# Optimization experiments

Measured on AMD Instinct MI355X. Metric: run time of the kernel, lower is better.

Reference implementation:

```python
import jax, jax.numpy as jnp
import numpy as np

H, DQS, DQP, DVS, DVP = 12, 16, 4, 16, 8
S_SCALAR = (3.0 * DQS) ** -0.5
S_POINT = (3.0 * DQP * (9.0 * 2.0 ** 0.5)) ** -0.5
S_PAIR = 3.0 ** -0.5
_OFF = np.cumsum([0, H * DQS, H * DQS, H * DVS, H * DQP * 3, H * DQP * 3, H * DVP * 3])


def _ln(x, g, b, eps=1e-5):
    mu = x.mean(-1, keepdims=True)
    var = x.var(-1, keepdims=True)
    return (x - mu) / jnp.sqrt(var + eps) * g + b


def setup_inputs() -> dict:
    B, N, D, PD = 2, 512, 384, 128
    key = jax.random.key(0)
    ks = jax.random.split(key, 12)
    node_feats = jax.random.normal(ks[0], (B, N, D), jnp.float32)
    pair_feats = jax.random.normal(ks[1], (B, N, N, PD), jnp.float32)
    mask = jnp.ones((B, N), dtype=bool)
    # random per-residue rigid frames (orthonormal rotations via QR)
    rot = jnp.linalg.qr(jax.random.normal(ks[2], (B, N, 3, 3), jnp.float32))[0]
    trans = jax.random.normal(ks[3], (B, N, 3), jnp.float32)
    dim_qkv = int(_OFF[-1])             # 1152
    dim_out = H * (PD + DVS + 4 * DVP)  # 2112
    s = 0.02
    p = dict(
        ln_s_g=jnp.ones((D,)), ln_s_b=jnp.zeros((D,)),
        ln_p_g=jnp.ones((PD,)), ln_p_b=jnp.zeros((PD,)),
        w_pair_bias=s * jax.random.normal(ks[4], (PD, H), jnp.float32),
        w_qkv=s * jax.random.normal(ks[5], (D, dim_qkv), jnp.float32),
        point_weights=jnp.full((1, H, 1, 1), float(np.log(np.e - 1.0)), jnp.float32),
        w_out=s * jax.random.normal(ks[6], (dim_out, D), jnp.float32),
        b_out=jnp.zeros((D,)),
        ln_t_g=jnp.ones((D,)), ln_t_b=jnp.zeros((D,)),
        w_ff1=s * jax.random.normal(ks[7], (D, 4 * D), jnp.float32),
        b_ff1=jnp.zeros((4 * D,)),
        w_ff2=s * jax.random.normal(ks[8], (4 * D, D), jnp.float32),
        b_ff2=jnp.zeros((D,)),
    )
    return dict(node_feats=node_feats, pair_feats=pair_feats, mask=mask,
                rot=rot, trans=trans, **p)


def reference(node_feats, pair_feats, mask, rot, trans,
              ln_s_g, ln_s_b, ln_p_g, ln_p_b, w_pair_bias, w_qkv,
              point_weights, w_out, b_out,
              ln_t_g, ln_t_b, w_ff1, b_ff1, w_ff2, b_ff2):
    b, n, d = node_feats.shape
    x = _ln(node_feats, ln_s_g, ln_s_b)
    p = _ln(pair_feats, ln_p_g, ln_p_b)
    pair_bias = jnp.einsum('bijd,dh->bhij', p, w_pair_bias)
    qkv = x @ w_qkv  # (b,n,1152)

    def heads(t, dh):
        return t.reshape(b, n, H, dh).transpose(0, 2, 1, 3)  # b h n d

    q_s = heads(qkv[..., _OFF[0]:_OFF[1]], DQS)
    k_s = heads(qkv[..., _OFF[1]:_OFF[2]], DQS)
    v_s = heads(qkv[..., _OFF[2]:_OFF[3]], DVS)

    def to_pts(t, dp):
        pts = t.reshape(b, n, H * dp, 3)
        # rigid apply: R_i @ x + t_i (global frame)
        pts = jnp.einsum('bnxy,bnpy->bnpx', rot, pts) + trans[:, :, None, :]
        return pts.reshape(b, n, H, dp, 3).transpose(0, 2, 1, 3, 4)  # b h n d 3

    q_p = to_pts(qkv[..., _OFF[3]:_OFF[4]], DQP)
    k_p = to_pts(qkv[..., _OFF[4]:_OFF[5]], DQP)
    v_p = to_pts(qkv[..., _OFF[5]:_OFF[6]], DVP)

    scalar_logits = jnp.einsum('bhid,bhjd->bhij', q_s, k_s)
    # dist attn: -sum_{d,c} (q-k)^2, expanded to avoid (b,h,n,n,d,3) intermediate
    qq = jnp.sum(q_p * q_p, axis=(-1, -2))
    kk = jnp.sum(k_p * k_p, axis=(-1, -2))
    qk = jnp.einsum('bhidc,bhjdc->bhij', q_p, k_p)
    point_logits = -(qq[..., :, None] + kk[..., None, :] - 2.0 * qk)
    point_logits = point_logits * jax.nn.softplus(point_weights)

    neg = jnp.finfo(node_feats.dtype).min
    pm = mask[:, None, :, None] & mask[:, None, None, :]  # b 1 i j
    scalar_logits = jnp.where(pm, scalar_logits, neg)
    point_logits = jnp.where(pm, point_logits, neg)
    pair_bias = jnp.where(pm, pair_bias, neg)

    logits = S_SCALAR * scalar_logits + S_POINT * point_logits + S_PAIR * pair_bias
    attn = jax.nn.softmax(logits, axis=-1)

    out_s = jnp.einsum('bhij,bhjd->bhid', attn, v_s)
    out_pair = jnp.einsum('bhij,bijd->bhid', attn, p)
    out_p = jnp.einsum('bhij,bhjdc->bhidc', attn, v_p)
    # rigid inverse: R_i^T (x - t_i) back to local frame
    pts = out_p.transpose(0, 2, 1, 3, 4).reshape(b, n, H * DVP, 3)
    pts = jnp.einsum('bnyx,bnpy->bnpx', rot, pts - trans[:, :, None, :])
    out_p = pts.reshape(b, n, H, DVP, 3)
    pnorm = jnp.sqrt(jnp.sum(out_p * out_p, axis=-1) + 1e-8)  # safe_norm

    cat = jnp.concatenate([
        out_s.transpose(0, 2, 1, 3).reshape(b, n, H * DVS),
        out_p.reshape(b, n, H * DVP * 3),
        pnorm.reshape(b, n, H * DVP),
        out_pair.transpose(0, 2, 1, 3).reshape(b, n, -1),
    ], axis=-1)
    attn_out = cat @ w_out + b_out

    # residuals + transition (dropout=0 -> identity). Note: transition is
    # applied to attn_out (pre-residual), exactly as in the torch forward.
    node1 = attn_out + node_feats
    t = _ln(attn_out, ln_t_g, ln_t_b)
    t = jax.nn.gelu(t @ w_ff1 + b_ff1) @ w_ff2 + b_ff2
    return t + node1
```

## Files before the change

kernel.cpp:

```cpp
#include <hip/hip_runtime.h>
#include <hip/hip_bf16.h>
#include <math.h>

typedef __hip_bfloat16 bf16;
typedef unsigned short ushort_t;
typedef ushort_t ushort8 __attribute__((ext_vector_type(8)));
typedef ushort_t us4 __attribute__((ext_vector_type(4)));
typedef short bf16x8 __attribute__((ext_vector_type(8)));
typedef float f32x4 __attribute__((ext_vector_type(4)));

constexpr float S_SCALAR = 0.14433756729740643f;
constexpr float S_POINT  = 0.08091531528f;
constexpr float S_PAIR   = 0.5773502691896258f;

__device__ inline float ldf(const float* p) { return *p; }
__device__ inline float ldf(const bf16* p)  { return __bfloat162float(*p); }
__device__ inline void stf(float* p, float v) { *p = v; }
__device__ inline void stf(bf16* p, float v)  { *p = __float2bfloat16(v); }

__device__ inline short f2bfs(float x) {
  return (short)__builtin_bit_cast(unsigned short, __float2bfloat16(x));
}
__device__ inline ushort_t f2bfu(float x) {
  return (ushort_t)__builtin_bit_cast(unsigned short, __float2bfloat16(x));
}

__device__ inline float gelu_tanh(float x) {
  float c = 0.7978845608028654f * (x + 0.044715f * x * x * x);
  return 0.5f * x * (1.f + tanhf(c));
}

__global__ __launch_bounds__(128) void ln384_kernel(
    const float* __restrict__ in, const float* __restrict__ g,
    const float* __restrict__ b, float* __restrict__ out)
{
  int row = blockIdx.x;
  const float* x = in + (size_t)row * 384;
  int t = threadIdx.x;
  float v[3]; float s = 0.f, s2 = 0.f;
#pragma unroll
  for (int i = 0; i < 3; i++) { v[i] = x[t + 128 * i]; s += v[i]; s2 += v[i] * v[i]; }
  for (int o = 32; o; o >>= 1) { s += __shfl_down(s, o); s2 += __shfl_down(s2, o); }
  __shared__ float sh[4];
  int wid = t >> 6, lane = t & 63;
  if (lane == 0) { sh[wid] = s; sh[2 + wid] = s2; }
  __syncthreads();
  s = sh[0] + sh[1]; s2 = sh[2] + sh[3];
  float mean = s * (1.f / 384.f);
  float var = s2 * (1.f / 384.f) - mean * mean;
  float rstd = rsqrtf(fmaxf(var, 0.f) + 1e-5f);
  float* orow = out + (size_t)row * 384;
#pragma unroll
  for (int i = 0; i < 3; i++) {
    int c = t + 128 * i;
    orow[c] = (v[i] - mean) * rstd * g[c] + b[c];
  }
}

__global__ __launch_bounds__(256) void prep_all_kernel(
    const float* __restrict__ w_qkv, const float* __restrict__ w_out,
    const float* __restrict__ w_ff1, const float* __restrict__ w_ff2,
    ushort_t* __restrict__ wqkvT, ushort_t* __restrict__ woutT,
    ushort_t* __restrict__ wff1T, ushort_t* __restrict__ wff2T,
    const float* __restrict__ g, const float* __restrict__ bb,
    const float* __restrict__ wpb, ushort_t* __restrict__ gwbT,
    float* __restrict__ gsbs)
{
  __shared__ float shmem[2048];
  int bid = blockIdx.x;
  int t = threadIdx.x;
  if (bid < 2376) {
    const float* src; ushort_t* dst; int K, N, bx, by;
    if (bid < 432)       { src = w_qkv; dst = wqkvT; K = 384;  N = 1152; bx = bid % 36;          by = bid / 36; }
    else if (bid < 1224) { src = w_out; dst = woutT; K = 2112; N = 384;  bx = (bid - 432) % 12;  by = (bid - 432) / 12; }
    else if (bid < 1800) { src = w_ff1; dst = wff1T; K = 384;  N = 1536; bx = (bid - 1224) % 48; by = (bid - 1224) / 48; }
    else                 { src = w_ff2; dst = wff2T; K = 1536; N = 384;  bx = (bid - 1800) % 12; by = (bid - 1800) / 12; }
    float (&tile)[32][33] = *reinterpret_cast<float (*)[32][33]>(shmem);
    int n0 = bx * 32, k0 = by * 32;
    int c = t & 31, r4 = (t >> 5) * 4;
#pragma unroll
    for (int i = 0; i < 4; i++)
      tile[r4 + i][c] = src[(size_t)(k0 + r4 + i) * N + n0 + c];
    __syncthreads();
#pragma unroll
    for (int i = 0; i < 4; i++)
      dst[(size_t)(n0 + r4 + i) * K + k0 + c] = f2bfu(tile[c][r4 + i]);
    return;
  }
  for (int idx = t; idx < 2048; idx += 256) {
    int h = idx >> 7, c = idx & 127;
    float v = (h < 12) ? g[c] * wpb[c * 12 + h] : 0.f;
    bf16 r = __float2bfloat16(v);
    gwbT[idx] = __builtin_bit_cast(unsigned short, r);
    shmem[idx] = __bfloat162float(r);
  }
  __syncthreads();
  if (t < 16) {
    float s = 0.f;
    for (int c = 0; c < 128; c++) s += shmem[t * 128 + c];
    gsbs[t] = s;
  } else if (t < 32) {
    int h = t - 16;
    float s = 0.f;
    if (h < 12) for (int c = 0; c < 128; c++) s = fmaf(bb[c], wpb[c * 12 + h], s);
    gsbs[t] = s;
  }
}

template <int EPI>
__global__ __launch_bounds__(256) void gemm_mfma_kernel(
    const float* __restrict__ A, const ushort_t* __restrict__ BT,
    const float* __restrict__ bias, const float* __restrict__ r1,
    const float* __restrict__ r2, float* __restrict__ C,
    int M, int Nn, int K)
{
  __shared__ ushort_t As[64][72];
  __shared__ ushort_t Bs[64][72];
  int t = threadIdx.x;
  int w = t >> 6, l = t & 63;
  int m0 = blockIdx.y * 64, n0 = blockIdx.x * 64;
  int wm = (w >> 1) * 32, wn = (w & 1) * 32;
  int lr = l & 15, lk = l >> 4;
  int sr = t >> 2, sc = (t & 3) * 16;
  f32x4 acc[2][2];
#pragma unroll
  for (int i = 0; i < 2; i++)
#pragma unroll
    for (int j = 0; j < 2; j++) acc[i][j] = (f32x4){0.f, 0.f, 0.f, 0.f};

  for (int k0 = 0; k0 < K; k0 += 64) {
    const float* Ar = A + (size_t)(m0 + sr) * K + k0 + sc;
    const ushort_t* Br = BT + (size_t)(n0 + sr) * K + k0 + sc;
    float4 a0 = *(const float4*)(Ar + 0);
    float4 a1 = *(const float4*)(Ar + 4);
    float4 a2 = *(const float4*)(Ar + 8);
    float4 a3 = *(const float4*)(Ar + 12);
    ushort8 b0 = *(const ushort8*)(Br + 0);
    ushort8 b1 = *(const ushort8*)(Br + 8);
    ushort8 u0, u1;
    u0[0] = f2bfu(a0.x); u0[1] = f2bfu(a0.y); u0[2] = f2bfu(a0.z); u0[3] = f2bfu(a0.w);
    u0[4] = f2bfu(a1.x); u0[5] = f2bfu(a1.y); u0[6] = f2bfu(a1.z); u0[7] = f2bfu(a1.w);
    u1[0] = f2bfu(a2.x); u1[1] = f2bfu(a2.y); u1[2] = f2bfu(a2.z); u1[3] = f2bfu(a2.w);
    u1[4] = f2bfu(a3.x); u1[5] = f2bfu(a3.y); u1[6] = f2bfu(a3.z); u1[7] = f2bfu(a3.w);
    *(ushort8*)&As[sr][sc] = u0;
    *(ushort8*)&As[sr][sc + 8] = u1;
    *(ushort8*)&Bs[sr][sc] = b0;
    *(ushort8*)&Bs[sr][sc + 8] = b1;
    __syncthreads();
#pragma unroll
    for (int kk = 0; kk < 2; kk++) {
      bf16x8 af0 = *(const bf16x8*)&As[wm + lr][kk * 32 + lk * 8];
      bf16x8 af1 = *(const bf16x8*)&As[wm + 16 + lr][kk * 32 + lk * 8];
      bf16x8 bf0 = *(const bf16x8*)&Bs[wn + lr][kk * 32 + lk * 8];
      bf16x8 bf1 = *(const bf16x8*)&Bs[wn + 16 + lr][kk * 32 + lk * 8];
      acc[0][0] = __builtin_amdgcn_mfma_f32_16x16x32_bf16(af0, bf0, acc[0][0], 0, 0, 0);
      acc[0][1] = __builtin_amdgcn_mfma_f32_16x16x32_bf16(af0, bf1, acc[0][1], 0, 0, 0);
      acc[1][0] = __builtin_amdgcn_mfma_f32_16x16x32_bf16(af1, bf0, acc[1][0], 0, 0, 0);
      acc[1][1] = __builtin_amdgcn_mfma_f32_16x16x32_bf16(af1, bf1, acc[1][1], 0, 0, 0);
    }
    __syncthreads();
  }
#pragma unroll
  for (int mf = 0; mf < 2; mf++) {
#pragma unroll
    for (int nf = 0; nf < 2; nf++) {
      int nn = n0 + wn + nf * 16 + lr;
      float bv = bias ? bias[nn] : 0.f;
#pragma unroll
      for (int e = 0; e < 4; e++) {
        int m = m0 + wm + mf * 16 + lk * 4 + e;
        float v = acc[mf][nf][e] + bv;
        if (EPI == 1) v = gelu_tanh(v);
        if (EPI == 2) v += r1[(size_t)m * Nn + nn] + r2[(size_t)m * Nn + nn];
        C[(size_t)m * Nn + nn] = v;
      }
    }
  }
}

__global__ __launch_bounds__(256) void points_kernel(
    const float* __restrict__ qkv, const float* __restrict__ rot,
    const float* __restrict__ trans, float* __restrict__ qpg,
    float* __restrict__ kpg, float* __restrict__ vpg,
    float* __restrict__ qq, float* __restrict__ kk)
{
  int bn = blockIdx.x;
  const float* row = qkv + (size_t)bn * 1152;
  __shared__ float R[9], T[3];
  __shared__ float qbuf[144], kbuf[144];
  int t = threadIdx.x;
  if (t < 9) R[t] = rot[bn * 9 + t];
  if (t >= 16 && t < 19) T[t - 16] = trans[bn * 3 + t - 16];
  __syncthreads();
  if (t < 192) {
    int base = (t < 48) ? (576 + t * 3) : (t < 96) ? (720 + (t - 48) * 3) : (864 + (t - 96) * 3);
    float x = row[base], y = row[base + 1], z = row[base + 2];
    float gx = R[0] * x + R[1] * y + R[2] * z + T[0];
    float gy = R[3] * x + R[4] * y + R[5] * z + T[1];
    float gz = R[6] * x + R[7] * y + R[8] * z + T[2];
    if (t < 48) {
      float* d = qpg + (size_t)bn * 144 + t * 3;
      d[0] = gx; d[1] = gy; d[2] = gz;
      qbuf[t * 3 + 0] = gx; qbuf[t * 3 + 1] = gy; qbuf[t * 3 + 2] = gz;
    } else if (t < 96) {
      int p = t - 48;
      float* d = kpg + (size_t)bn * 144 + p * 3;
      d[0] = gx; d[1] = gy; d[2] = gz;
      kbuf[p * 3 + 0] = gx; kbuf[p * 3 + 1] = gy; kbuf[p * 3 + 2] = gz;
    } else {
      int p = t - 96;
      float* d = vpg + (size_t)bn * 288 + p * 3;
      d[0] = gx; d[1] = gy; d[2] = gz;
    }
  }
  __syncthreads();
  if (t < 24) {
    int h = (t < 12) ? t : t - 12;
    const float* src = (t < 12) ? qbuf : kbuf;
    float ssum = 0.f;
#pragma unroll
    for (int d = 0; d < 12; d++) { float v = src[h * 12 + d]; ssum = fmaf(v, v, ssum); }
    if (t < 12) qq[bn * 12 + h] = ssum; else kk[bn * 12 + h] = ssum;
  }
}

__global__ __launch_bounds__(256) void kv_prep_kernel(
    const float* __restrict__ qkv, const float* __restrict__ kpg,
    const float* __restrict__ kk, const float* __restrict__ vpg,
    float* __restrict__ kpackT, ushort_t* __restrict__ vT)
{
  int bh = blockIdx.x;
  int b = bh / 12, h = bh - b * 12;
  int j = blockIdx.y * 256 + threadIdx.x;
  const float* row = qkv + (size_t)(b * 512 + j) * 1152;
  float* kt = kpackT + (size_t)bh * 29 * 512;
#pragma unroll
  for (int d = 0; d < 16; d++) kt[d * 512 + j] = row[192 + h * 16 + d];
  const float* kp = kpg + (size_t)(b * 512 + j) * 144 + h * 12;
#pragma unroll
  for (int d = 0; d < 12; d++) kt[(16 + d) * 512 + j] = kp[d];
  kt[28 * 512 + j] = kk[(b * 512 + j) * 12 + h];
  ushort_t* vt = vT + (size_t)bh * 40 * 512;
#pragma unroll
  for (int c = 0; c < 16; c++) vt[c * 512 + j] = f2bfu(row[384 + h * 16 + c]);
  const float* vp = vpg + (size_t)(b * 512 + j) * 288 + h * 24;
#pragma unroll
  for (int c = 0; c < 24; c++) vt[(16 + c) * 512 + j] = f2bfu(vp[c]);
}

__global__ __launch_bounds__(256) void pair_bias_kernel(
    const float* __restrict__ pair, const ushort_t* __restrict__ gwbT,
    const float* __restrict__ gsbs, bf16* __restrict__ bias,
    float* __restrict__ meanb, float* __restrict__ rstdb)
{
  int t = threadIdx.x;
  int wv = t >> 6, l = t & 63;
  int lr = l & 15, lk = l >> 4;
  size_t rid0 = (size_t)blockIdx.x * 128 + (size_t)wv * 32;

  bf16x8 bfrag[4];
#pragma unroll
  for (int kc = 0; kc < 4; kc++) {
    const ushort_t* gp = gwbT + lr * 128 + kc * 32 + lk * 8;
    us4 q0 = *(const us4*)gp;
    us4 q1 = *(const us4*)(gp + 4);
    bfrag[kc][0] = (short)q0[0]; bfrag[kc][1] = (short)q0[1];
    bfrag[kc][2] = (short)q0[2]; bfrag[kc][3] = (short)q0[3];
    bfrag[kc][4] = (short)q1[0]; bfrag[kc][5] = (short)q1[1];
    bfrag[kc][6] = (short)q1[2]; bfrag[kc][7] = (short)q1[3];
  }

  const float* p0 = pair + (rid0 + lr) * 128 + lk * 8;
  f32x4 acc0 = {0.f, 0.f, 0.f, 0.f}, acc1 = {0.f, 0.f, 0.f, 0.f};
  float s0 = 0.f, s20 = 0.f, s1 = 0.f, s21 = 0.f;
#pragma unroll
  for (int kc = 0; kc < 4; kc++) {
    float4 u0 = *(const float4*)(p0 + kc * 32);
    float4 u1 = *(const float4*)(p0 + kc * 32 + 4);
    float4 w0 = *(const float4*)(p0 + 2048 + kc * 32);
    float4 w1 = *(const float4*)(p0 + 2048 + kc * 32 + 4);
    s0 += u0.x + u0.y + u0.z + u0.w + u1.x + u1.y + u1.z + u1.w;
    s20 = fmaf(u0.x, u0.x, s20); s20 = fmaf(u0.y, u0.y, s20);
    s20 = fmaf(u0.z, u0.z, s20); s20 = fmaf(u0.w, u0.w, s20);
    s20 = fmaf(u1.x, u1.x, s20); s20 = fmaf(u1.y, u1.y, s20);
    s20 = fmaf(u1.z, u1.z, s20); s20 = fmaf(u1.w, u1.w, s20);
    s1 += w0.x + w0.y + w0.z + w0.w + w1.x + w1.y + w1.z + w1.w;
    s21 = fmaf(w0.x, w0.x, s21); s21 = fmaf(w0.y, w0.y, s21);
    s21 = fmaf(w0.z, w0.z, s21); s21 = fmaf(w0.w, w0.w, s21);
    s21 = fmaf(w1.x, w1.x, s21); s21 = fmaf(w1.y, w1.y, s21);
    s21 = fmaf(w1.z, w1.z, s21); s21 = fmaf(w1.w, w1.w, s21);
    bf16x8 a0, a1;
    a0[0] = f2bfs(u0.x); a0[1] = f2bfs(u0.y); a0[2] = f2bfs(u0.z); a0[3] = f2bfs(u0.w);
    a0[4] = f2bfs(u1.x); a0[5] = f2bfs(u1.y); a0[6] = f2bfs(u1.z); a0[7] = f2bfs(u1.w);
    a1[0] = f2bfs(w0.x); a1[1] = f2bfs(w0.y); a1[2] = f2bfs(w0.z); a1[3] = f2bfs(w0.w);
    a1[4] = f2bfs(w1.x); a1[5] = f2bfs(w1.y); a1[6] = f2bfs(w1.z); a1[7] = f2bfs(w1.w);
    acc0 = __builtin_amdgcn_mfma_f32_16x16x32_bf16(a0, bfrag[kc], acc0, 0, 0, 0);
    acc1 = __builtin_amdgcn_mfma_f32_16x16x32_bf16(a1, bfrag[kc], acc1, 0, 0, 0);
  }
  s0 += __shfl_xor(s0, 16);  s0 += __shfl_xor(s0, 32);
  s20 += __shfl_xor(s20, 16); s20 += __shfl_xor(s20, 32);
  s1 += __shfl_xor(s1, 16);  s1 += __shfl_xor(s1, 32);
  s21 += __shfl_xor(s21, 16); s21 += __shfl_xor(s21, 32);
  float mean0 = s0 * (1.f / 128.f);
  float rstd0 = rsqrtf(fmaxf(s20 * (1.f / 128.f) - mean0 * mean0, 0.f) + 1e-5f);
  float mean1 = s1 * (1.f / 128.f);
  float rstd1 = rsqrtf(fmaxf(s21 * (1.f / 128.f) - mean1 * mean1, 0.f) + 1e-5f);
  if (lk == 0) {
    meanb[rid0 + lr] = mean0;      rstdb[rid0 + lr] = rstd0;
    meanb[rid0 + 16 + lr] = mean1; rstdb[rid0 + 16 + lr] = rstd1;
  }
  float gsum = gsbs[lr], bsum = gsbs[16 + lr];
  int b = (int)(rid0 >> 18);
  int i = (int)((rid0 >> 9) & 511);
  int j0 = (int)(rid0 & 511);
  us4 pk0, pk1;
#pragma unroll
  for (int e = 0; e < 4; e++) {
    int r = lk * 4 + e;
    float m0 = __shfl(mean0, r), rs0 = __shfl(rstd0, r);
    float m1 = __shfl(mean1, r), rs1 = __shfl(rstd1, r);
    pk0[e] = (ushort_t)(unsigned short)f2bfs(rs0 * (acc0[e] - m0 * gsum) + bsum);
    pk1[e] = (ushort_t)(unsigned short)f2bfs(rs1 * (acc1[e] - m1 * gsum) + bsum);
  }
  if (lr < 12) {
    ushort_t* dst = (ushort_t*)bias + ((size_t)(b * 12 + lr) * 512 + i) * 512 + j0 + lk * 4;
    *(us4*)dst = pk0;
    *(us4*)(dst + 16) = pk1;
  }
}

__global__ __launch_bounds__(256) void attn_kernel(
    const float* __restrict__ qkv, const float* __restrict__ qpg,
    const float* __restrict__ qq, const float* __restrict__ kpackT,
    const bf16* __restrict__ bias, const float* __restrict__ pw,
    bf16* __restrict__ attn)
{
  int bx = blockIdx.x;
  int i = bx & 511;
  int bh = bx >> 9;
  int b = bh / 12;
  int h = bh - b * 12;
  int t = threadIdx.x;
  __shared__ float qs[16], qp[12], sc[2], redm[4], reds[4];
  const float* qrow = qkv + (size_t)(b * 512 + i) * 1152;
  if (t < 16) qs[t] = qrow[h * 16 + t];
  if (t >= 16 && t < 28) qp[t - 16] = qpg[(size_t)(b * 512 + i) * 144 + h * 12 + (t - 16)];
  if (t == 28) sc[0] = qq[(b * 512 + i) * 12 + h];
  if (t == 29) sc[1] = log1pf(__expf(pw[h]));
  __syncthreads();
  float qqi = sc[0], sp = sc[1];
  const bf16* biasrow = bias + (size_t)bx * 512;
  const float* kT = kpackT + (size_t)bh * 29 * 512;
  float lg[2]; float lmax = -3.0e38f;
#pragma unroll
  for (int r = 0; r < 2; r++) {
    int j = t + 256 * r;
    float sdot = 0.f;
#pragma unroll
    for (int d = 0; d < 16; d++) sdot = fmaf(qs[d], kT[d * 512 + j], sdot);
    float pdot = 0.f;
#pragma unroll
    for (int d = 0; d < 12; d++) pdot = fmaf(qp[d], kT[(16 + d) * 512 + j], pdot);
    float kkj = kT[28 * 512 + j];
    float l = S_SCALAR * sdot + S_POINT * sp * (2.f * pdot - qqi - kkj) + S_PAIR * ldf(biasrow + j);
    lg[r] = l;
    lmax = fmaxf(lmax, l);
  }
  int wid = t >> 6, lane = t & 63;
  for (int o = 32; o; o >>= 1) lmax = fmaxf(lmax, __shfl_down(lmax, o));
  if (lane == 0) redm[wid] = lmax;
  __syncthreads();
  float Mx = fmaxf(fmaxf(redm[0], redm[1]), fmaxf(redm[2], redm[3]));
  float e0 = __expf(lg[0] - Mx), e1 = __expf(lg[1] - Mx);
  float ssum = e0 + e1;
  for (int o = 32; o; o >>= 1) ssum += __shfl_down(ssum, o);
  if (lane == 0) reds[wid] = ssum;
  __syncthreads();
  float inv = 1.f / (reds[0] + reds[1] + reds[2] + reds[3]);
  bf16* arow = attn + ((size_t)(b * 512 + i) * 12 + h) * 512;
  stf(arow + t, e0 * inv);
  stf(arow + t + 256, e1 * inv);
}

__global__ __launch_bounds__(256) void pair_attn_kernel(
    const float* __restrict__ pair, const float* __restrict__ meanb,
    const float* __restrict__ rstdb, const float* __restrict__ g,
    const float* __restrict__ bb, const bf16* __restrict__ attn,
    float* __restrict__ cat)
{
  int bn = blockIdx.x;
  const float4* prow = (const float4*)(pair + (size_t)bn * 512 * 128);
  const bf16* arow = attn + (size_t)bn * 12 * 512;
  __shared__ float ap[6144];
  __shared__ float mu[512];
  __shared__ float gl[128], bl[128];
  int t = threadIdx.x;
  if (t < 128) { gl[t] = g[t]; bl[t] = bb[t]; }
  for (int j = t; j < 512; j += 256) mu[j] = meanb[(size_t)bn * 512 + j];
  for (int idx = t; idx < 6144; idx += 256) {
    int h = idx >> 9, j = idx & 511;
    ap[j * 12 + h] = ldf(arow + idx) * rstdb[(size_t)bn * 512 + j];
  }
  __syncthreads();

  int tc = t & 31, tj = t >> 5;
  float acc[12][4];
#pragma unroll
  for (int h = 0; h < 12; h++)
#pragma unroll
    for (int c = 0; c < 4; c++) acc[h][c] = 0.f;

  for (int it = 0; it < 32; it++) {
    int jb = it * 16;
#pragma unroll
    for (int s = 0; s < 2; s++) {
      int jj = jb + tj * 2 + s;
      float4 pv = prow[(size_t)jj * 32 + tc];
      float m = mu[jj];
      pv.x -= m; pv.y -= m; pv.z -= m; pv.w -= m;
      const float4* apr = (const float4*)&ap[jj * 12];
      float4 a0 = apr[0], a1 = apr[1], a2 = apr[2];
      acc[0][0] = fmaf(a0.x, pv.x, acc[0][0]); acc[0][1] = fmaf(a0.x, pv.y, acc[0][1]);
      acc[0][2] = fmaf(a0.x, pv.z, acc[0][2]); acc[0][3] = fmaf(a0.x, pv.w, acc[0][3]);
      acc[1][0] = fmaf(a0.y, pv.x, acc[1][0]); acc[1][1] = fmaf(a0.y, pv.y, acc[1][1]);
      acc[1][2] = fmaf(a0.y, pv.z, acc[1][2]); acc[1][3] = fmaf(a0.y, pv.w, acc[1][3]);
      acc[2][0] = fmaf(a0.z, pv.x, acc[2][0]); acc[2][1] = fmaf(a0.z, pv.y, acc[2][1]);
      acc[2][2] = fmaf(a0.z, pv.z, acc[2][2]); acc[2][3] = fmaf(a0.z, pv.w, acc[2][3]);
      acc[3][0] = fmaf(a0.w, pv.x, acc[3][0]); acc[3][1] = fmaf(a0.w, pv.y, acc[3][1]);
      acc[3][2] = fmaf(a0.w, pv.z, acc[3][2]); acc[3][3] = fmaf(a0.w, pv.w, acc[3][3]);
      acc[4][0] = fmaf(a1.x, pv.x, acc[4][0]); acc[4][1] = fmaf(a1.x, pv.y, acc[4][1]);
      acc[4][2] = fmaf(a1.x, pv.z, acc[4][2]); acc[4][3] = fmaf(a1.x, pv.w, acc[4][3]);
      acc[5][0] = fmaf(a1.y, pv.x, acc[5][0]); acc[5][1] = fmaf(a1.y, pv.y, acc[5][1]);
      acc[5][2] = fmaf(a1.y, pv.z, acc[5][2]); acc[5][3] = fmaf(a1.y, pv.w, acc[5][3]);
      acc[6][0] = fmaf(a1.z, pv.x, acc[6][0]); acc[6][1] = fmaf(a1.z, pv.y, acc[6][1]);
      acc[6][2] = fmaf(a1.z, pv.z, acc[6][2]); acc[6][3] = fmaf(a1.z, pv.w, acc[6][3]);
      acc[7][0] = fmaf(a1.w, pv.x, acc[7][0]); acc[7][1] = fmaf(a1.w, pv.y, acc[7][1]);
      acc[7][2] = fmaf(a1.w, pv.z, acc[7][2]); acc[7][3] = fmaf(a1.w, pv.w, acc[7][3]);
      acc[8][0] = fmaf(a2.x, pv.x, acc[8][0]); acc[8][1] = fmaf(a2.x, pv.y, acc[8][1]);
      acc[8][2] = fmaf(a2.x, pv.z, acc[8][2]); acc[8][3] = fmaf(a2.x, pv.w, acc[8][3]);
      acc[9][0] = fmaf(a2.y, pv.x, acc[9][0]); acc[9][1] = fmaf(a2.y, pv.y, acc[9][1]);
      acc[9][2] = fmaf(a2.y, pv.z, acc[9][2]); acc[9][3] = fmaf(a2.y, pv.w, acc[9][3]);
      acc[10][0] = fmaf(a2.z, pv.x, acc[10][0]); acc[10][1] = fmaf(a2.z, pv.y, acc[10][1]);
      acc[10][2] = fmaf(a2.z, pv.z, acc[10][2]); acc[10][3] = fmaf(a2.z, pv.w, acc[10][3]);
      acc[11][0] = fmaf(a2.w, pv.x, acc[11][0]); acc[11][1] = fmaf(a2.w, pv.y, acc[11][1]);
      acc[11][2] = fmaf(a2.w, pv.z, acc[11][2]); acc[11][3] = fmaf(a2.w, pv.w, acc[11][3]);
    }
  }
  __syncthreads();
#pragma unroll
  for (int h = 0; h < 12; h++)
#pragma unroll
    for (int c = 0; c < 4; c++) acc[h][c] += __shfl_down(acc[h][c], 32);
  int w = t >> 6, lane = t & 63;
  if (lane < 32) {
#pragma unroll
    for (int h = 0; h < 12; h++)
      *(float4*)&ap[(w * 12 + h) * 128 + tc * 4] = *(float4*)&acc[h][0];
  }
  __syncthreads();
  float* crow = cat + (size_t)bn * 2112 + 576;
  for (int idx = t; idx < 1536; idx += 256) {
    int c = idx & 127;
    float P = ap[idx] + ap[1536 + idx] + ap[3072 + idx] + ap[4608 + idx];
    crow[idx] = fmaf(P, gl[c], bl[c]);
  }
}

__global__ __launch_bounds__(256) void sv_gemm_kernel(
    const bf16* __restrict__ attn, const ushort_t* __restrict__ vT,
    float* __restrict__ svraw)
{
  int i0 = blockIdx.x * 64;
  int bh = blockIdx.y;
  int b = bh / 12, h = bh - b * 12;
  __shared__ ushort_t As_[64][72];
  __shared__ ushort_t Bs_[48][72];
  int t = threadIdx.x;
  int w = t >> 6, l = t & 63, lr = l & 15, lk = l >> 4;
  int ai = t >> 2, as = (t & 3) * 16;
  const ushort_t* ab = (const ushort_t*)attn;
  const ushort_t* vbase = vT + (size_t)bh * 40 * 512;
  f32x4 acc[3];
#pragma unroll
  for (int n = 0; n < 3; n++) acc[n] = (f32x4){0.f, 0.f, 0.f, 0.f};

  for (int jt = 0; jt < 8; jt++) {
    int jb = jt * 64;
    size_t aoff = ((size_t)(b * 512 + i0 + ai) * 12 + h) * 512 + jb + as;
    ushort8 a0 = *(const ushort8*)(ab + aoff);
    ushort8 a1 = *(const ushort8*)(ab + aoff + 8);
    *(ushort8*)&As_[ai][as] = a0;
    *(ushort8*)&As_[ai][as + 8] = a1;
    for (int idx = t; idx < 384; idx += 256) {
      int c = idx >> 3, j8 = (idx & 7) * 8;
      ushort8 v = {0, 0, 0, 0, 0, 0, 0, 0};
      if (c < 40) v = *(const ushort8*)(vbase + (size_t)c * 512 + jb + j8);
      *(ushort8*)&Bs_[c][j8] = v;
    }
    __syncthreads();
#pragma unroll
    for (int kk = 0; kk < 2; kk++) {
      bf16x8 af = *(const bf16x8*)&As_[w * 16 + lr][kk * 32 + lk * 8];
#pragma unroll
      for (int n = 0; n < 3; n++) {
        bf16x8 bf_ = *(const bf16x8*)&Bs_[n * 16 + lr][kk * 32 + lk * 8];
        acc[n] = __builtin_amdgcn_mfma_f32_16x16x32_bf16(af, bf_, acc[n], 0, 0, 0);
      }
    }
    __syncthreads();
  }
#pragma unroll
  for (int n = 0; n < 3; n++) {
    int c = n * 16 + lr;
    if (c < 40) {
#pragma unroll
      for (int e = 0; e < 4; e++) {
        int i = i0 + w * 16 + lk * 4 + e;
        svraw[(size_t)(b * 512 + i) * 480 + h * 40 + c] = acc[n][e];
      }
    }
  }
}

__global__ __launch_bounds__(192) void sv_epilogue_kernel(
    const float* __restrict__ svraw, const float* __restrict__ rot,
    const float* __restrict__ trans, float* __restrict__ cat)
{
  int bn = blockIdx.x;
  const float* sv = svraw + (size_t)bn * 480;
  float* crow = cat + (size_t)bn * 2112;
  int t = threadIdx.x;
  {
    int h2 = t >> 4, d = t & 15;
    crow[t] = sv[h2 * 40 + d];
  }
  if (t < 96) {
    int h2 = t >> 3, dp = t & 7;
    float T0 = trans[bn * 3], T1 = trans[bn * 3 + 1], T2 = trans[bn * 3 + 2];
    const float* R = rot + bn * 9;
    float px = sv[h2 * 40 + 16 + dp * 3 + 0] - T0;
    float py = sv[h2 * 40 + 16 + dp * 3 + 1] - T1;
    float pz = sv[h2 * 40 + 16 + dp * 3 + 2] - T2;
    float lx = R[0] * px + R[3] * py + R[6] * pz;
    float ly = R[1] * px + R[4] * py + R[7] * pz;
    float lz = R[2] * px + R[5] * py + R[8] * pz;
    crow[192 + h2 * 24 + dp * 3 + 0] = lx;
    crow[192 + h2 * 24 + dp * 3 + 1] = ly;
    crow[192 + h2 * 24 + dp * 3 + 2] = lz;
    crow[480 + h2 * 8 + dp] = sqrtf(lx * lx + ly * ly + lz * lz + 1e-8f);
  }
}

extern "C" void kernel_launch(void* const* d_in, const int* in_sizes, int n_in,
                              void* d_out, int out_size, void* d_ws, size_t ws_size,
                              hipStream_t stream)
{
  const float* node   = (const float*)d_in[0];
  const float* pair   = (const float*)d_in[1];
  const float* rot    = (const float*)d_in[3];
  const float* trans  = (const float*)d_in[4];
  const float* ln_s_g = (const float*)d_in[5];
  const float* ln_s_b = (const float*)d_in[6];
  const float* ln_p_g = (const float*)d_in[7];
  const float* ln_p_b = (const float*)d_in[8];
  const float* wpb    = (const float*)d_in[9];
  const float* w_qkv  = (const float*)d_in[10];
  const float* pw     = (const float*)d_in[11];
  const float* w_out  = (const float*)d_in[12];
  const float* b_out  = (const float*)d_in[13];
  const float* ln_t_g = (const float*)d_in[14];
  const float* ln_t_b = (const float*)d_in[15];
  const float* w_ff1  = (const float*)d_in[16];
  const float* b_ff1  = (const float*)d_in[17];
  const float* w_ff2  = (const float*)d_in[18];
  const float* b_ff2  = (const float*)d_in[19];
  float* out = (float*)d_out;
  float* ws = (float*)d_ws;

  float* qkv   = ws;
  float* qpg   = ws + 1179648;
  float* kpg   = ws + 1327104;
  float* vpg   = ws + 1474560;
  float* qq    = ws + 1769472;
  float* kk    = ws + 1781760;
  float* meanb = ws + 1794048;
  float* svraw = meanb;
  float* rstdb = ws + 2318336;
  float* x     = ws + 2842624;
  float* tn    = x;
  float* ao    = ws + 3235840;
  bf16*  biasb = (bf16*)(ws + 3629056);
  float* cat   = ws + 3629056;
  bf16*  attnb = (bf16*)(ws + 6774784);
  float* gb    = ws + 6774784;
  ushort_t* gwbT = (ushort_t*)(ws + 9920512);
  float* gsbs  = ws + 9921536;
  ushort_t* wqkvT = (ushort_t*)(ws + 9921568);
  ushort_t* woutT = (ushort_t*)(ws + 10142752);
  ushort_t* wff1T = (ushort_t*)(ws + 10548256);
  ushort_t* wff2T = (ushort_t*)(ws + 10843168);
  float* kpackT = ws + 11138080;
  ushort_t* vT  = (ushort_t*)(ws + 11494432);

  prep_all_kernel<<<2377, 256, 0, stream>>>(w_qkv, w_out, w_ff1, w_ff2,
      wqkvT, woutT, wff1T, wff2T, ln_p_g, ln_p_b, wpb, gwbT, gsbs);
  ln384_kernel<<<1024, 128, 0, stream>>>(node, ln_s_g, ln_s_b, x);
  gemm_mfma_kernel<0><<<dim3(18, 16), 256, 0, stream>>>(x, wqkvT, nullptr, nullptr, nullptr, qkv, 1024, 1152, 384);
  points_kernel<<<1024, 256, 0, stream>>>(qkv, rot, trans, qpg, kpg, vpg, qq, kk);
  kv_prep_kernel<<<dim3(24, 2), 256, 0, stream>>>(qkv, kpg, kk, vpg, kpackT, vT);
  pair_bias_kernel<<<4096, 256, 0, stream>>>(pair, gwbT, gsbs, biasb, meanb, rstdb);
  attn_kernel<<<12288, 256, 0, stream>>>(qkv, qpg, qq, kpackT, biasb, pw, attnb);
  pair_attn_kernel<<<1024, 256, 0, stream>>>(pair, meanb, rstdb, ln_p_g, ln_p_b, attnb, cat);
  sv_gemm_kernel<<<dim3(8, 24), 256, 0, stream>>>(attnb, vT, svraw);
  sv_epilogue_kernel<<<1024, 192, 0, stream>>>(svraw, rot, trans, cat);
  gemm_mfma_kernel<0><<<dim3(6, 16), 256, 0, stream>>>(cat, woutT, b_out, nullptr, nullptr, ao, 1024, 384, 2112);
  ln384_kernel<<<1024, 128, 0, stream>>>(ao, ln_t_g, ln_t_b, tn);
  gemm_mfma_kernel<1><<<dim3(24, 16), 256, 0, stream>>>(tn, wff1T, b_ff1, nullptr, nullptr, gb, 1024, 1536, 384);
  gemm_mfma_kernel<2><<<dim3(6, 16), 256, 0, stream>>>(gb, wff2T, b_ff2, ao, node, out, 1024, 384, 1536);
}
```

Baseline: 619.3 us.

## Rework attention pipeline with fp16 MFMA logits, pair-out GEMM, fused prep kernels

Replaces the per-row scalar attention kernel with a 64-row tiled kernel that computes scalar and point logits in one fp16 MFMA dot product. Q is prescaled and zero-padded to 32 dims and K packs the points, while the -q² term is dropped because softmax ignores a per-row constant. The pair-bias kernel now writes a normalized fp16 transposed pair slab, so the pair-weighted output becomes an MFMA GEMM fused with the SV epilogue. The points and kv-prep kernels merge into one, and the first layernorm is folded into the weight-prep launch. Moving attention weights and V from bf16 to fp16 changes precision and range, and the large extra pnT buffer adds memory traffic.

```diff
diff --git a/kernel.cpp b/kernel.cpp
--- a/kernel.cpp
+++ b/kernel.cpp
@@ -3,10 +3,12 @@
 #include <math.h>
 
 typedef __hip_bfloat16 bf16;
+typedef _Float16 f16;
 typedef unsigned short ushort_t;
 typedef ushort_t ushort8 __attribute__((ext_vector_type(8)));
 typedef ushort_t us4 __attribute__((ext_vector_type(4)));
 typedef short bf16x8 __attribute__((ext_vector_type(8)));
+typedef f16 f16x8 __attribute__((ext_vector_type(8)));
 typedef float f32x4 __attribute__((ext_vector_type(4)));
 
 constexpr float S_SCALAR = 0.14433756729740643f;
@@ -14,15 +16,19 @@
 constexpr float S_PAIR   = 0.5773502691896258f;
 
 __device__ inline float ldf(const float* p) { return *p; }
-__device__ inline float ldf(const bf16* p)  { return __bfloat162float(*p); }
 __device__ inline void stf(float* p, float v) { *p = v; }
-__device__ inline void stf(bf16* p, float v)  { *p = __float2bfloat16(v); }
 
 __device__ inline short f2bfs(float x) {
   return (short)__builtin_bit_cast(unsigned short, __float2bfloat16(x));
 }
 __device__ inline ushort_t f2bfu(float x) {
   return (ushort_t)__builtin_bit_cast(unsigned short, __float2bfloat16(x));
+}
+__device__ inline ushort_t f2hu(float x) {
+  return __builtin_bit_cast(ushort_t, (f16)x);
+}
+__device__ inline float h2f(ushort_t u) {
+  return (float)__builtin_bit_cast(f16, u);
 }
 
 __device__ inline float gelu_tanh(float x) {
@@ -64,7 +70,9 @@
     ushort_t* __restrict__ wff1T, ushort_t* __restrict__ wff2T,
     const float* __restrict__ g, const float* __restrict__ bb,
     const float* __restrict__ wpb, ushort_t* __restrict__ gwbT,
-    float* __restrict__ gsbs)
+    float* __restrict__ gsbs,
+    const float* __restrict__ node, const float* __restrict__ ln_s_g,
+    const float* __restrict__ ln_s_b, float* __restrict__ xout)
 {
   __shared__ float shmem[2048];
   int bid = blockIdx.x;
@@ -87,23 +95,47 @@
       dst[(size_t)(n0 + r4 + i) * K + k0 + c] = f2bfu(tile[c][r4 + i]);
     return;
   }
-  for (int idx = t; idx < 2048; idx += 256) {
-    int h = idx >> 7, c = idx & 127;
-    float v = (h < 12) ? g[c] * wpb[c * 12 + h] : 0.f;
-    bf16 r = __float2bfloat16(v);
-    gwbT[idx] = __builtin_bit_cast(unsigned short, r);
-    shmem[idx] = __bfloat162float(r);
-  }
+  if (bid == 2376) {
+    for (int idx = t; idx < 2048; idx += 256) {
+      int h = idx >> 7, c = idx & 127;
+      float v = (h < 12) ? g[c] * wpb[c * 12 + h] : 0.f;
+      bf16 r = __float2bfloat16(v);
+      gwbT[idx] = __builtin_bit_cast(unsigned short, r);
+      shmem[idx] = __bfloat162float(r);
+    }
+    __syncthreads();
+    if (t < 16) {
+      float s = 0.f;
+      for (int c = 0; c < 128; c++) s += shmem[t * 128 + c];
+      gsbs[t] = s;
+    } else if (t < 32) {
+      int h = t - 16;
+      float s = 0.f;
+      if (h < 12) for (int c = 0; c < 128; c++) s = fmaf(bb[c], wpb[c * 12 + h], s);
+      gsbs[t] = s;
+    }
+    return;
+  }
+  int half = t >> 7, tt = t & 127;
+  int row = (bid - 2377) * 2 + half;
+  const float* x = node + (size_t)row * 384;
+  float v[3]; float s = 0.f, s2 = 0.f;
+#pragma unroll
+  for (int i = 0; i < 3; i++) { v[i] = x[tt + 128 * i]; s += v[i]; s2 += v[i] * v[i]; }
+  for (int o = 32; o; o >>= 1) { s += __shfl_down(s, o); s2 += __shfl_down(s2, o); }
+  int wid = t >> 6, lane = t & 63;
+  if (lane == 0) { shmem[wid] = s; shmem[4 + wid] = s2; }
   __syncthreads();
-  if (t < 16) {
-    float s = 0.f;
-    for (int c = 0; c < 128; c++) s += shmem[t * 128 + c];
-    gsbs[t] = s;
-  } else if (t < 32) {
-    int h = t - 16;
-    float s = 0.f;
-    if (h < 12) for (int c = 0; c < 128; c++) s = fmaf(bb[c], wpb[c * 12 + h], s);
-    gsbs[t] = s;
+  s = shmem[half * 2] + shmem[half * 2 + 1];
+  s2 = shmem[4 + half * 2] + shmem[4 + half * 2 + 1];
+  float mean = s * (1.f / 384.f);
+  float var = s2 * (1.f / 384.f) - mean * mean;
+  float rstd = rsqrtf(fmaxf(var, 0.f) + 1e-5f);
+  float* orow = xout + (size_t)row * 384;
+#pragma unroll
+  for (int i = 0; i < 3; i++) {
+    int c = tt + 128 * i;
+    orow[c] = (v[i] - mean) * rstd * ln_s_g[c] + ln_s_b[c];
   }
 }
 
@@ -178,80 +210,70 @@
   }
 }
 
-__global__ __launch_bounds__(256) void points_kernel(
+__global__ __launch_bounds__(256) void qkv_post_kernel(
     const float* __restrict__ qkv, const float* __restrict__ rot,
-    const float* __restrict__ trans, float* __restrict__ qpg,
-    float* __restrict__ kpg, float* __restrict__ vpg,
-    float* __restrict__ qq, float* __restrict__ kk)
-{
-  int bn = blockIdx.x;
-  const float* row = qkv + (size_t)bn * 1152;
-  __shared__ float R[9], T[3];
-  __shared__ float qbuf[144], kbuf[144];
-  int t = threadIdx.x;
-  if (t < 9) R[t] = rot[bn * 9 + t];
-  if (t >= 16 && t < 19) T[t - 16] = trans[bn * 3 + t - 16];
-  __syncthreads();
-  if (t < 192) {
-    int base = (t < 48) ? (576 + t * 3) : (t < 96) ? (720 + (t - 48) * 3) : (864 + (t - 96) * 3);
-    float x = row[base], y = row[base + 1], z = row[base + 2];
-    float gx = R[0] * x + R[1] * y + R[2] * z + T[0];
-    float gy = R[3] * x + R[4] * y + R[5] * z + T[1];
-    float gz = R[6] * x + R[7] * y + R[8] * z + T[2];
-    if (t < 48) {
-      float* d = qpg + (size_t)bn * 144 + t * 3;
-      d[0] = gx; d[1] = gy; d[2] = gz;
-      qbuf[t * 3 + 0] = gx; qbuf[t * 3 + 1] = gy; qbuf[t * 3 + 2] = gz;
-    } else if (t < 96) {
-      int p = t - 48;
-      float* d = kpg + (size_t)bn * 144 + p * 3;
-      d[0] = gx; d[1] = gy; d[2] = gz;
-      kbuf[p * 3 + 0] = gx; kbuf[p * 3 + 1] = gy; kbuf[p * 3 + 2] = gz;
-    } else {
-      int p = t - 96;
-      float* d = vpg + (size_t)bn * 288 + p * 3;
-      d[0] = gx; d[1] = gy; d[2] = gz;
-    }
-  }
-  __syncthreads();
-  if (t < 24) {
-    int h = (t < 12) ? t : t - 12;
-    const float* src = (t < 12) ? qbuf : kbuf;
-    float ssum = 0.f;
-#pragma unroll
-    for (int d = 0; d < 12; d++) { float v = src[h * 12 + d]; ssum = fmaf(v, v, ssum); }
-    if (t < 12) qq[bn * 12 + h] = ssum; else kk[bn * 12 + h] = ssum;
-  }
-}
-
-__global__ __launch_bounds__(256) void kv_prep_kernel(
-    const float* __restrict__ qkv, const float* __restrict__ kpg,
-    const float* __restrict__ kk, const float* __restrict__ vpg,
-    float* __restrict__ kpackT, ushort_t* __restrict__ vT)
+    const float* __restrict__ trans, const float* __restrict__ pw,
+    f16* __restrict__ qhat, f16* __restrict__ khat,
+    float* __restrict__ kkb, ushort_t* __restrict__ vT)
 {
   int bh = blockIdx.x;
   int b = bh / 12, h = bh - b * 12;
   int j = blockIdx.y * 256 + threadIdx.x;
-  const float* row = qkv + (size_t)(b * 512 + j) * 1152;
-  float* kt = kpackT + (size_t)bh * 29 * 512;
-#pragma unroll
-  for (int d = 0; d < 16; d++) kt[d * 512 + j] = row[192 + h * 16 + d];
-  const float* kp = kpg + (size_t)(b * 512 + j) * 144 + h * 12;
-#pragma unroll
-  for (int d = 0; d < 12; d++) kt[(16 + d) * 512 + j] = kp[d];
-  kt[28 * 512 + j] = kk[(b * 512 + j) * 12 + h];
+  int bn = b * 512 + j;
+  const float* row = qkv + (size_t)bn * 1152;
+  float R[9];
+#pragma unroll
+  for (int k = 0; k < 9; k++) R[k] = rot[bn * 9 + k];
+  float T0 = trans[bn * 3], T1 = trans[bn * 3 + 1], T2 = trans[bn * 3 + 2];
+  float sp = log1pf(__expf(pw[h]));
+  float c1 = 2.f * S_POINT * sp;
+  f16* qh = qhat + ((size_t)bh * 512 + j) * 32;
+  f16* kh = khat + ((size_t)bh * 512 + j) * 32;
+#pragma unroll
+  for (int d = 0; d < 16; d++) {
+    qh[d] = (f16)(S_SCALAR * row[h * 16 + d]);
+    kh[d] = (f16)(row[192 + h * 16 + d]);
+  }
+#pragma unroll
+  for (int p = 0; p < 4; p++) {
+    int base = 576 + (h * 4 + p) * 3;
+    float x = row[base], y = row[base + 1], z = row[base + 2];
+    qh[16 + p * 3 + 0] = (f16)(c1 * (R[0] * x + R[1] * y + R[2] * z + T0));
+    qh[16 + p * 3 + 1] = (f16)(c1 * (R[3] * x + R[4] * y + R[5] * z + T1));
+    qh[16 + p * 3 + 2] = (f16)(c1 * (R[6] * x + R[7] * y + R[8] * z + T2));
+  }
+  float kksum = 0.f;
+#pragma unroll
+  for (int p = 0; p < 4; p++) {
+    int base = 720 + (h * 4 + p) * 3;
+    float x = row[base], y = row[base + 1], z = row[base + 2];
+    float gx = R[0] * x + R[1] * y + R[2] * z + T0;
+    float gy = R[3] * x + R[4] * y + R[5] * z + T1;
+    float gz = R[6] * x + R[7] * y + R[8] * z + T2;
+    kh[16 + p * 3 + 0] = (f16)gx; kh[16 + p * 3 + 1] = (f16)gy; kh[16 + p * 3 + 2] = (f16)gz;
+    kksum = fmaf(gx, gx, kksum); kksum = fmaf(gy, gy, kksum); kksum = fmaf(gz, gz, kksum);
+  }
+#pragma unroll
+  for (int d = 28; d < 32; d++) { qh[d] = (f16)0.f; kh[d] = (f16)0.f; }
+  kkb[(size_t)bh * 512 + j] = kksum;
   ushort_t* vt = vT + (size_t)bh * 40 * 512;
 #pragma unroll
-  for (int c = 0; c < 16; c++) vt[c * 512 + j] = f2bfu(row[384 + h * 16 + c]);
-  const float* vp = vpg + (size_t)(b * 512 + j) * 288 + h * 24;
-#pragma unroll
-  for (int c = 0; c < 24; c++) vt[(16 + c) * 512 + j] = f2bfu(vp[c]);
+  for (int c = 0; c < 16; c++) vt[c * 512 + j] = f2hu(row[384 + h * 16 + c]);
+#pragma unroll
+  for (int p = 0; p < 8; p++) {
+    int base = 864 + (h * 8 + p) * 3;
+    float x = row[base], y = row[base + 1], z = row[base + 2];
+    vt[(16 + p * 3 + 0) * 512 + j] = f2hu(R[0] * x + R[1] * y + R[2] * z + T0);
+    vt[(16 + p * 3 + 1) * 512 + j] = f2hu(R[3] * x + R[4] * y + R[5] * z + T1);
+    vt[(16 + p * 3 + 2) * 512 + j] = f2hu(R[6] * x + R[7] * y + R[8] * z + T2);
+  }
 }
 
 __global__ __launch_bounds__(256) void pair_bias_kernel(
     const float* __restrict__ pair, const ushort_t* __restrict__ gwbT,
-    const float* __restrict__ gsbs, bf16* __restrict__ bias,
-    float* __restrict__ meanb, float* __restrict__ rstdb)
+    const float* __restrict__ gsbs, const float* __restrict__ g,
+    const float* __restrict__ bb, ushort_t* __restrict__ bias,
+    f16* __restrict__ pnT)
 {
   int t = threadIdx.x;
   int wv = t >> 6, l = t & 63;
@@ -305,10 +327,33 @@
   float rstd0 = rsqrtf(fmaxf(s20 * (1.f / 128.f) - mean0 * mean0, 0.f) + 1e-5f);
   float mean1 = s1 * (1.f / 128.f);
   float rstd1 = rsqrtf(fmaxf(s21 * (1.f / 128.f) - mean1 * mean1, 0.f) + 1e-5f);
-  if (lk == 0) {
-    meanb[rid0 + lr] = mean0;      rstdb[rid0 + lr] = rstd0;
-    meanb[rid0 + 16 + lr] = mean1; rstdb[rid0 + 16 + lr] = rstd1;
-  }
+
+  int slab = (int)(rid0 >> 9);
+  int j0w = (int)(rid0 & 511);
+  f16* sl = pnT + (size_t)slab * 65536;
+  int ju = j0w + lr, jw = j0w + 16 + lr;
+#pragma unroll
+  for (int kc = 0; kc < 4; kc++) {
+    int c0 = kc * 32 + lk * 8;
+    float4 u0 = *(const float4*)(p0 + kc * 32);
+    float4 u1 = *(const float4*)(p0 + kc * 32 + 4);
+    float4 w0 = *(const float4*)(p0 + 2048 + kc * 32);
+    float4 w1 = *(const float4*)(p0 + 2048 + kc * 32 + 4);
+    float4 g0 = *(const float4*)(g + c0);
+    float4 g1 = *(const float4*)(g + c0 + 4);
+    float4 b0 = *(const float4*)(bb + c0);
+    float4 b1 = *(const float4*)(bb + c0 + 4);
+    float uu[8] = {u0.x, u0.y, u0.z, u0.w, u1.x, u1.y, u1.z, u1.w};
+    float ww[8] = {w0.x, w0.y, w0.z, w0.w, w1.x, w1.y, w1.z, w1.w};
+    float gg[8] = {g0.x, g0.y, g0.z, g0.w, g1.x, g1.y, g1.z, g1.w};
+    float bv[8] = {b0.x, b0.y, b0.z, b0.w, b1.x, b1.y, b1.z, b1.w};
+#pragma unroll
+    for (int e = 0; e < 8; e++) {
+      sl[(size_t)(c0 + e) * 512 + ju] = (f16)(fmaf((uu[e] - mean0) * rstd0, gg[e], bv[e]));
+      sl[(size_t)(c0 + e) * 512 + jw] = (f16)(fmaf((ww[e] - mean1) * rstd1, gg[e], bv[e]));
+    }
+  }
+
   float gsum = gsbs[lr], bsum = gsbs[16 + lr];
   int b = (int)(rid0 >> 18);
   int i = (int)((rid0 >> 9) & 511);
@@ -319,155 +364,84 @@
     int r = lk * 4 + e;
     float m0 = __shfl(mean0, r), rs0 = __shfl(rstd0, r);
     float m1 = __shfl(mean1, r), rs1 = __shfl(rstd1, r);
-    pk0[e] = (ushort_t)(unsigned short)f2bfs(rs0 * (acc0[e] - m0 * gsum) + bsum);
-    pk1[e] = (ushort_t)(unsigned short)f2bfs(rs1 * (acc1[e] - m1 * gsum) + bsum);
+    pk0[e] = f2hu(rs0 * (acc0[e] - m0 * gsum) + bsum);
+    pk1[e] = f2hu(rs1 * (acc1[e] - m1 * gsum) + bsum);
   }
   if (lr < 12) {
-    ushort_t* dst = (ushort_t*)bias + ((size_t)(b * 12 + lr) * 512 + i) * 512 + j0 + lk * 4;
+    ushort_t* dst = bias + ((size_t)(b * 12 + lr) * 512 + i) * 512 + j0 + lk * 4;
     *(us4*)dst = pk0;
     *(us4*)(dst + 16) = pk1;
   }
 }
 
-__global__ __launch_bounds__(256) void attn_kernel(
-    const float* __restrict__ qkv, const float* __restrict__ qpg,
-    const float* __restrict__ qq, const float* __restrict__ kpackT,
-    const bf16* __restrict__ bias, const float* __restrict__ pw,
-    bf16* __restrict__ attn)
-{
-  int bx = blockIdx.x;
-  int i = bx & 511;
-  int bh = bx >> 9;
-  int b = bh / 12;
-  int h = bh - b * 12;
+__global__ __launch_bounds__(256, 1) void attn_kernel(
+    const f16* __restrict__ qhat, const f16* __restrict__ khat,
+    const float* __restrict__ kkb, const ushort_t* __restrict__ bias,
+    const float* __restrict__ pw, ushort_t* __restrict__ attn)
+{
+  int i0 = blockIdx.x * 64;
+  int bh = blockIdx.y;
+  int b = bh / 12, h = bh - b * 12;
   int t = threadIdx.x;
-  __shared__ float qs[16], qp[12], sc[2], redm[4], reds[4];
-  const float* qrow = qkv + (size_t)(b * 512 + i) * 1152;
-  if (t < 16) qs[t] = qrow[h * 16 + t];
-  if (t >= 16 && t < 28) qp[t - 16] = qpg[(size_t)(b * 512 + i) * 144 + h * 12 + (t - 16)];
-  if (t == 28) sc[0] = qq[(b * 512 + i) * 12 + h];
-  if (t == 29) sc[1] = log1pf(__expf(pw[h]));
-  __syncthreads();
-  float qqi = sc[0], sp = sc[1];
-  const bf16* biasrow = bias + (size_t)bx * 512;
-  const float* kT = kpackT + (size_t)bh * 29 * 512;
-  float lg[2]; float lmax = -3.0e38f;
-#pragma unroll
-  for (int r = 0; r < 2; r++) {
-    int j = t + 256 * r;
-    float sdot = 0.f;
-#pragma unroll
-    for (int d = 0; d < 16; d++) sdot = fmaf(qs[d], kT[d * 512 + j], sdot);
-    float pdot = 0.f;
-#pragma unroll
-    for (int d = 0; d < 12; d++) pdot = fmaf(qp[d], kT[(16 + d) * 512 + j], pdot);
-    float kkj = kT[28 * 512 + j];
-    float l = S_SCALAR * sdot + S_POINT * sp * (2.f * pdot - qqi - kkj) + S_PAIR * ldf(biasrow + j);
-    lg[r] = l;
-    lmax = fmaxf(lmax, l);
-  }
-  int wid = t >> 6, lane = t & 63;
-  for (int o = 32; o; o >>= 1) lmax = fmaxf(lmax, __shfl_down(lmax, o));
-  if (lane == 0) redm[wid] = lmax;
-  __syncthreads();
-  float Mx = fmaxf(fmaxf(redm[0], redm[1]), fmaxf(redm[2], redm[3]));
-  float e0 = __expf(lg[0] - Mx), e1 = __expf(lg[1] - Mx);
-  float ssum = e0 + e1;
-  for (int o = 32; o; o >>= 1) ssum += __shfl_down(ssum, o);
-  if (lane == 0) reds[wid] = ssum;
-  __syncthreads();
-  float inv = 1.f / (reds[0] + reds[1] + reds[2] + reds[3]);
-  bf16* arow = attn + ((size_t)(b * 512 + i) * 12 + h) * 512;
-  stf(arow + t, e0 * inv);
-  stf(arow + t + 256, e1 * inv);
-}
-
-__global__ __launch_bounds__(256) void pair_attn_kernel(
-    const float* __restrict__ pair, const float* __restrict__ meanb,
-    const float* __restrict__ rstdb, const float* __restrict__ g,
-    const float* __restrict__ bb, const bf16* __restrict__ attn,
-    float* __restrict__ cat)
-{
-  int bn = blockIdx.x;
-  const float4* prow = (const float4*)(pair + (size_t)bn * 512 * 128);
-  const bf16* arow = attn + (size_t)bn * 12 * 512;
-  __shared__ float ap[6144];
-  __shared__ float mu[512];
-  __shared__ float gl[128], bl[128];
-  int t = threadIdx.x;
-  if (t < 128) { gl[t] = g[t]; bl[t] = bb[t]; }
-  for (int j = t; j < 512; j += 256) mu[j] = meanb[(size_t)bn * 512 + j];
-  for (int idx = t; idx < 6144; idx += 256) {
-    int h = idx >> 9, j = idx & 511;
-    ap[j * 12 + h] = ldf(arow + idx) * rstdb[(size_t)bn * 512 + j];
-  }
-  __syncthreads();
-
-  int tc = t & 31, tj = t >> 5;
-  float acc[12][4];
-#pragma unroll
-  for (int h = 0; h < 12; h++)
-#pragma unroll
-    for (int c = 0; c < 4; c++) acc[h][c] = 0.f;
-
-  for (int it = 0; it < 32; it++) {
-    int jb = it * 16;
-#pragma unroll
-    for (int s = 0; s < 2; s++) {
-      int jj = jb + tj * 2 + s;
-      float4 pv = prow[(size_t)jj * 32 + tc];
-      float m = mu[jj];
-      pv.x -= m; pv.y -= m; pv.z -= m; pv.w -= m;
-      const float4* apr = (const float4*)&ap[jj * 12];
-      float4 a0 = apr[0], a1 = apr[1], a2 = apr[2];
-      acc[0][0] = fmaf(a0.x, pv.x, acc[0][0]); acc[0][1] = fmaf(a0.x, pv.y, acc[0][1]);
-      acc[0][2] = fmaf(a0.x, pv.z, acc[0][2]); acc[0][3] = fmaf(a0.x, pv.w, acc[0][3]);
-      acc[1][0] = fmaf(a0.y, pv.x, acc[1][0]); acc[1][1] = fmaf(a0.y, pv.y, acc[1][1]);
-      acc[1][2] = fmaf(a0.y, pv.z, acc[1][2]); acc[1][3] = fmaf(a0.y, pv.w, acc[1][3]);
-      acc[2][0] = fmaf(a0.z, pv.x, acc[2][0]); acc[2][1] = fmaf(a0.z, pv.y, acc[2][1]);
-      acc[2][2] = fmaf(a0.z, pv.z, acc[2][2]); acc[2][3] = fmaf(a0.z, pv.w, acc[2][3]);
-      acc[3][0] = fmaf(a0.w, pv.x, acc[3][0]); acc[3][1] = fmaf(a0.w, pv.y, acc[3][1]);
-      acc[3][2] = fmaf(a0.w, pv.z, acc[3][2]); acc[3][3] = fmaf(a0.w, pv.w, acc[3][3]);
-      acc[4][0] = fmaf(a1.x, pv.x, acc[4][0]); acc[4][1] = fmaf(a1.x, pv.y, acc[4][1]);
-      acc[4][2] = fmaf(a1.x, pv.z, acc[4][2]); acc[4][3] = fmaf(a1.x, pv.w, acc[4][3]);
-      acc[5][0] = fmaf(a1.y, pv.x, acc[5][0]); acc[5][1] = fmaf(a1.y, pv.y, acc[5][1]);
-      acc[5][2] = fmaf(a1.y, pv.z, acc[5][2]); acc[5][3] = fmaf(a1.y, pv.w, acc[5][3]);
-      acc[6][0] = fmaf(a1.z, pv.x, acc[6][0]); acc[6][1] = fmaf(a1.z, pv.y, acc[6][1]);
-      acc[6][2] = fmaf(a1.z, pv.z, acc[6][2]); acc[6][3] = fmaf(a1.z, pv.w, acc[6][3]);
-      acc[7][0] = fmaf(a1.w, pv.x, acc[7][0]); acc[7][1] = fmaf(a1.w, pv.y, acc[7][1]);
-      acc[7][2] = fmaf(a1.w, pv.z, acc[7][2]); acc[7][3] = fmaf(a1.w, pv.w, acc[7][3]);
-      acc[8][0] = fmaf(a2.x, pv.x, acc[8][0]); acc[8][1] = fmaf(a2.x, pv.y, acc[8][1]);
-      acc[8][2] = fmaf(a2.x, pv.z, acc[8][2]); acc[8][3] = fmaf(a2.x, pv.w, acc[8][3]);
-      acc[9][0] = fmaf(a2.y, pv.x, acc[9][0]); acc[9][1] = fmaf(a2.y, pv.y, acc[9][1]);
-      acc[9][2] = fmaf(a2.y, pv.z, acc[9][2]); acc[9][3] = fmaf(a2.y, pv.w, acc[9][3]);
-      acc[10][0] = fmaf(a2.z, pv.x, acc[10][0]); acc[10][1] = fmaf(a2.z, pv.y, acc[10][1]);
-      acc[10][2] = fmaf(a2.z, pv.z, acc[10][2]); acc[10][3] = fmaf(a2.z, pv.w, acc[10][3]);
-      acc[11][0] = fmaf(a2.w, pv.x, acc[11][0]); acc[11][1] = fmaf(a2.w, pv.y, acc[11][1]);
-      acc[11][2] = fmaf(a2.w, pv.z, acc[11][2]); acc[11][3] = fmaf(a2.w, pv.w, acc[11][3]);
-    }
-  }
-  __syncthreads();
-#pragma unroll
-  for (int h = 0; h < 12; h++)
-#pragma unroll
-    for (int c = 0; c < 4; c++) acc[h][c] += __shfl_down(acc[h][c], 32);
-  int w = t >> 6, lane = t & 63;
-  if (lane < 32) {
-#pragma unroll
-    for (int h = 0; h < 12; h++)
-      *(float4*)&ap[(w * 12 + h) * 128 + tc * 4] = *(float4*)&acc[h][0];
-  }
-  __syncthreads();
-  float* crow = cat + (size_t)bn * 2112 + 576;
-  for (int idx = t; idx < 1536; idx += 256) {
-    int c = idx & 127;
-    float P = ap[idx] + ap[1536 + idx] + ap[3072 + idx] + ap[4608 + idx];
-    crow[idx] = fmaf(P, gl[c], bl[c]);
-  }
+  int w = t >> 6, l = t & 63, lr = l & 15, lk = l >> 4;
+  float spp = S_POINT * log1pf(__expf(pw[h]));
+  int iw0 = i0 + w * 16;
+  f16x8 afrag = *(const f16x8*)(qhat + ((size_t)bh * 512 + iw0 + lr) * 32 + lk * 8);
+  const f16* kbase = khat + (size_t)bh * 512 * 32;
+  const float* kkrow = kkb + (size_t)bh * 512;
+  const ushort_t* brow = bias + (size_t)bh * 512 * 512;
+  float lg[32][4];
+  float pmax[4] = {-3.0e38f, -3.0e38f, -3.0e38f, -3.0e38f};
+#pragma unroll
+  for (int jt = 0; jt < 32; jt++) {
+    int j = jt * 16 + lr;
+    f16x8 bfrag = *(const f16x8*)(kbase + (size_t)j * 32 + lk * 8);
+    f32x4 c = {0.f, 0.f, 0.f, 0.f};
+    c = __builtin_amdgcn_mfma_f32_16x16x32_f16(afrag, bfrag, c, 0, 0, 0);
+    float kkv = kkrow[j];
+#pragma unroll
+    for (int e = 0; e < 4; e++) {
+      int i = iw0 + lk * 4 + e;
+      float lv = c[e] + S_PAIR * h2f(brow[(size_t)i * 512 + j]) - spp * kkv;
+      lg[jt][e] = lv;
+      pmax[e] = fmaxf(pmax[e], lv);
+    }
+  }
+#pragma unroll
+  for (int e = 0; e < 4; e++) {
+    pmax[e] = fmaxf(pmax[e], __shfl_xor(pmax[e], 1));
+    pmax[e] = fmaxf(pmax[e], __shfl_xor(pmax[e], 2));
+    pmax[e] = fmaxf(pmax[e], __shfl_xor(pmax[e], 4));
+    pmax[e] = fmaxf(pmax[e], __shfl_xor(pmax[e], 8));
+  }
+  float ssum[4] = {0.f, 0.f, 0.f, 0.f};
+#pragma unroll
+  for (int jt = 0; jt < 32; jt++)
+#pragma unroll
+    for (int e = 0; e < 4; e++) {
+      float p = __expf(lg[jt][e] - pmax[e]);
+      lg[jt][e] = p;
+      ssum[e] += p;
+    }
+#pragma unroll
+  for (int e = 0; e < 4; e++) {
+    ssum[e] += __shfl_xor(ssum[e], 1);
+    ssum[e] += __shfl_xor(ssum[e], 2);
+    ssum[e] += __shfl_xor(ssum[e], 4);
+    ssum[e] += __shfl_xor(ssum[e], 8);
+    ssum[e] = 1.f / ssum[e];
+  }
+#pragma unroll
+  for (int jt = 0; jt < 32; jt++)
+#pragma unroll
+    for (int e = 0; e < 4; e++) {
+      int i = iw0 + lk * 4 + e;
+      attn[((size_t)(b * 512 + i) * 12 + h) * 512 + jt * 16 + lr] = f2hu(lg[jt][e] * ssum[e]);
+    }
 }
 
 __global__ __launch_bounds__(256) void sv_gemm_kernel(
-    const bf16* __restrict__ attn, const ushort_t* __restrict__ vT,
+    const ushort_t* __restrict__ attn, const ushort_t* __restrict__ vT,
     float* __restrict__ svraw)
 {
   int i0 = blockIdx.x * 64;
@@ -478,7 +452,6 @@
   int t = threadIdx.x;
   int w = t >> 6, l = t & 63, lr = l & 15, lk = l >> 4;
   int ai = t >> 2, as = (t & 3) * 16;
-  const ushort_t* ab = (const ushort_t*)attn;
   const ushort_t* vbase = vT + (size_t)bh * 40 * 512;
   f32x4 acc[3];
 #pragma unroll
@@ -487,8 +460,8 @@
   for (int jt = 0; jt < 8; jt++) {
     int jb = jt * 64;
     size_t aoff = ((size_t)(b * 512 + i0 + ai) * 12 + h) * 512 + jb + as;
-    ushort8 a0 = *(const ushort8*)(ab + aoff);
-    ushort8 a1 = *(const ushort8*)(ab + aoff + 8);
+    ushort8 a0 = *(const ushort8*)(attn + aoff);
+    ushort8 a1 = *(const ushort8*)(attn + aoff + 8);
     *(ushort8*)&As_[ai][as] = a0;
     *(ushort8*)&As_[ai][as + 8] = a1;
     for (int idx = t; idx < 384; idx += 256) {
@@ -500,11 +473,11 @@
     __syncthreads();
 #pragma unroll
     for (int kk = 0; kk < 2; kk++) {
-      bf16x8 af = *(const bf16x8*)&As_[w * 16 + lr][kk * 32 + lk * 8];
+      f16x8 af = *(const f16x8*)&As_[w * 16 + lr][kk * 32 + lk * 8];
 #pragma unroll
       for (int n = 0; n < 3; n++) {
-        bf16x8 bf_ = *(const bf16x8*)&Bs_[n * 16 + lr][kk * 32 + lk * 8];
-        acc[n] = __builtin_amdgcn_mfma_f32_16x16x32_bf16(af, bf_, acc[n], 0, 0, 0);
+        f16x8 bf_ = *(const f16x8*)&Bs_[n * 16 + lr][kk * 32 + lk * 8];
+        acc[n] = __builtin_amdgcn_mfma_f32_16x16x32_f16(af, bf_, acc[n], 0, 0, 0);
       }
     }
     __syncthreads();
@@ -522,32 +495,56 @@
   }
 }
 
-__global__ __launch_bounds__(192) void sv_epilogue_kernel(
+__global__ __launch_bounds__(256) void pair_out_kernel(
+    const ushort_t* __restrict__ attn, const f16* __restrict__ pnT,
     const float* __restrict__ svraw, const float* __restrict__ rot,
     const float* __restrict__ trans, float* __restrict__ cat)
 {
   int bn = blockIdx.x;
+  int t = threadIdx.x;
   const float* sv = svraw + (size_t)bn * 480;
   float* crow = cat + (size_t)bn * 2112;
-  int t = threadIdx.x;
-  {
+  if (t < 192) {
     int h2 = t >> 4, d = t & 15;
     crow[t] = sv[h2 * 40 + d];
-  }
-  if (t < 96) {
-    int h2 = t >> 3, dp = t & 7;
-    float T0 = trans[bn * 3], T1 = trans[bn * 3 + 1], T2 = trans[bn * 3 + 2];
-    const float* R = rot + bn * 9;
-    float px = sv[h2 * 40 + 16 + dp * 3 + 0] - T0;
-    float py = sv[h2 * 40 + 16 + dp * 3 + 1] - T1;
-    float pz = sv[h2 * 40 + 16 + dp * 3 + 2] - T2;
-    float lx = R[0] * px + R[3] * py + R[6] * pz;
-    float ly = R[1] * px + R[4] * py + R[7] * pz;
-    float lz = R[2] * px + R[5] * py + R[8] * pz;
-    crow[192 + h2 * 24 + dp * 3 + 0] = lx;
-    crow[192 + h2 * 24 + dp * 3 + 1] = ly;
-    crow[192 + h2 * 24 + dp * 3 + 2] = lz;
-    crow[480 + h2 * 8 + dp] = sqrtf(lx * lx + ly * ly + lz * lz + 1e-8f);
+    if (t < 96) {
+      int h3 = t >> 3, dp = t & 7;
+      float T0 = trans[bn * 3], T1 = trans[bn * 3 + 1], T2 = trans[bn * 3 + 2];
+      const float* R = rot + bn * 9;
+      float px = sv[h3 * 40 + 16 + dp * 3 + 0] - T0;
+      float py = sv[h3 * 40 + 16 + dp * 3 + 1] - T1;
+      float pz = sv[h3 * 40 + 16 + dp * 3 + 2] - T2;
+      float lx = R[0] * px + R[3] * py + R[6] * pz;
+      float ly = R[1] * px + R[4] * py + R[7] * pz;
+      float lz = R[2] * px + R[5] * py + R[8] * pz;
+      crow[192 + h3 * 24 + dp * 3 + 0] = lx;
+      crow[192 + h3 * 24 + dp * 3 + 1] = ly;
+      crow[192 + h3 * 24 + dp * 3 + 2] = lz;
+      crow[480 + h3 * 8 + dp] = sqrtf(lx * lx + ly * ly + lz * lz + 1e-8f);
+    }
+  }
+  int w = t >> 6, l = t & 63, lr = l & 15, lk = l >> 4;
+  const ushort_t* arow = attn + (size_t)bn * 12 * 512;
+  int ar = (lr < 12) ? lr : 11;
+  const f16* slab = pnT + (size_t)bn * 65536;
+  int n0 = w * 32;
+  f32x4 acc0 = {0.f, 0.f, 0.f, 0.f}, acc1 = {0.f, 0.f, 0.f, 0.f};
+#pragma unroll
+  for (int ks = 0; ks < 16; ks++) {
+    int kb = ks * 32 + lk * 8;
+    f16x8 af = *(const f16x8*)((const f16*)arow + (size_t)ar * 512 + kb);
+    f16x8 b0 = *(const f16x8*)(slab + (size_t)(n0 + lr) * 512 + kb);
+    f16x8 b1 = *(const f16x8*)(slab + (size_t)(n0 + 16 + lr) * 512 + kb);
+    acc0 = __builtin_amdgcn_mfma_f32_16x16x32_f16(af, b0, acc0, 0, 0, 0);
+    acc1 = __builtin_amdgcn_mfma_f32_16x16x32_f16(af, b1, acc1, 0, 0, 0);
+  }
+#pragma unroll
+  for (int e = 0; e < 4; e++) {
+    int hh = lk * 4 + e;
+    if (hh < 12) {
+      crow[576 + hh * 128 + n0 + lr] = acc0[e];
+      crow[576 + hh * 128 + n0 + 16 + lr] = acc1[e];
+    }
   }
 }
 
@@ -577,42 +574,36 @@
   float* out = (float*)d_out;
   float* ws = (float*)d_ws;
 
-  float* qkv   = ws;
-  float* qpg   = ws + 1179648;
-  float* kpg   = ws + 1327104;
-  float* vpg   = ws + 1474560;
-  float* qq    = ws + 1769472;
-  float* kk    = ws + 1781760;
-  float* meanb = ws + 1794048;
-  float* svraw = meanb;
-  float* rstdb = ws + 2318336;
-  float* x     = ws + 2842624;
-  float* tn    = x;
-  float* ao    = ws + 3235840;
-  bf16*  biasb = (bf16*)(ws + 3629056);
-  float* cat   = ws + 3629056;
-  bf16*  attnb = (bf16*)(ws + 6774784);
-  float* gb    = ws + 6774784;
-  ushort_t* gwbT = (ushort_t*)(ws + 9920512);
-  float* gsbs  = ws + 9921536;
-  ushort_t* wqkvT = (ushort_t*)(ws + 9921568);
-  ushort_t* woutT = (ushort_t*)(ws + 10142752);
-  ushort_t* wff1T = (ushort_t*)(ws + 10548256);
-  ushort_t* wff2T = (ushort_t*)(ws + 10843168);
-  float* kpackT = ws + 11138080;
-  ushort_t* vT  = (ushort_t*)(ws + 11494432);
-
-  prep_all_kernel<<<2377, 256, 0, stream>>>(w_qkv, w_out, w_ff1, w_ff2,
-      wqkvT, woutT, wff1T, wff2T, ln_p_g, ln_p_b, wpb, gwbT, gsbs);
-  ln384_kernel<<<1024, 128, 0, stream>>>(node, ln_s_g, ln_s_b, x);
+  float* qkv    = ws;
+  float* x      = ws + 1179648;
+  float* tn     = x;
+  float* ao     = ws + 1572864;
+  float* svraw  = ws + 1966080;
+  ushort_t* biasb = (ushort_t*)(ws + 2457600);
+  float* cat    = ws + 2457600;
+  ushort_t* attnb = (ushort_t*)(ws + 5603328);
+  float* gb     = ws + 5603328;
+  ushort_t* gwbT = (ushort_t*)(ws + 8749056);
+  float* gsbs   = ws + 8750080;
+  ushort_t* wqkvT = (ushort_t*)(ws + 8750112);
+  ushort_t* woutT = (ushort_t*)(ws + 8971296);
+  ushort_t* wff1T = (ushort_t*)(ws + 9376800);
+  ushort_t* wff2T = (ushort_t*)(ws + 9671712);
+  f16* qhat     = (f16*)(ws + 9966624);
+  f16* khat     = (f16*)(ws + 10163232);
+  float* kkb    = ws + 10359840;
+  ushort_t* vT  = (ushort_t*)(ws + 10372128);
+  f16* pnT      = (f16*)(ws + 10617888);
+
+  prep_all_kernel<<<2889, 256, 0, stream>>>(w_qkv, w_out, w_ff1, w_ff2,
+      wqkvT, woutT, wff1T, wff2T, ln_p_g, ln_p_b, wpb, gwbT, gsbs,
+      node, ln_s_g, ln_s_b, x);
   gemm_mfma_kernel<0><<<dim3(18, 16), 256, 0, stream>>>(x, wqkvT, nullptr, nullptr, nullptr, qkv, 1024, 1152, 384);
-  points_kernel<<<1024, 256, 0, stream>>>(qkv, rot, trans, qpg, kpg, vpg, qq, kk);
-  kv_prep_kernel<<<dim3(24, 2), 256, 0, stream>>>(qkv, kpg, kk, vpg, kpackT, vT);
-  pair_bias_kernel<<<4096, 256, 0, stream>>>(pair, gwbT, gsbs, biasb, meanb, rstdb);
-  attn_kernel<<<12288, 256, 0, stream>>>(qkv, qpg, qq, kpackT, biasb, pw, attnb);
-  pair_attn_kernel<<<1024, 256, 0, stream>>>(pair, meanb, rstdb, ln_p_g, ln_p_b, attnb, cat);
+  qkv_post_kernel<<<dim3(24, 2), 256, 0, stream>>>(qkv, rot, trans, pw, qhat, khat, kkb, vT);
+  pair_bias_kernel<<<4096, 256, 0, stream>>>(pair, gwbT, gsbs, ln_p_g, ln_p_b, biasb, pnT);
+  attn_kernel<<<dim3(8, 24), 256, 0, stream>>>(qhat, khat, kkb, biasb, pw, attnb);
   sv_gemm_kernel<<<dim3(8, 24), 256, 0, stream>>>(attnb, vT, svraw);
-  sv_epilogue_kernel<<<1024, 192, 0, stream>>>(svraw, rot, trans, cat);
+  pair_out_kernel<<<1024, 256, 0, stream>>>(attnb, pnT, svraw, rot, trans, cat);
   gemm_mfma_kernel<0><<<dim3(6, 16), 256, 0, stream>>>(cat, woutT, b_out, nullptr, nullptr, ao, 1024, 384, 2112);
   ln384_kernel<<<1024, 128, 0, stream>>>(ao, ln_t_g, ln_t_b, tn);
   gemm_mfma_kernel<1><<<dim3(24, 16), 256, 0, stream>>>(tn, wff1T, b_ff1, nullptr, nullptr, gb, 1024, 1536, 384);
```

After: 632.8 us. 1.02x slower.
